# Performance work log

Hardware: AMD Instinct MI355X
Metric: run time of the kernel (lower is better)

Reference implementation:

```python
import jax, jax.numpy as jnp
import numpy as np

N_HEADS = 16
HEAD_DIM = 64
D_MODEL = N_HEADS * HEAD_DIM  # 1024


def setup_inputs() -> dict:
    key = jax.random.key(0)
    ks = jax.random.split(key, 6)
    B, S, D = 2, 2048, D_MODEL
    s = 0.02
    return {
        "hidden_states": jax.random.normal(ks[0], (B, S, D), jnp.float32),
        "position_bias": jax.random.normal(ks[1], (1, N_HEADS, S, S), jnp.float32),
        "Wq": jax.random.normal(ks[2], (D, D), jnp.float32) * s,
        "Wk": jax.random.normal(ks[3], (D, D), jnp.float32) * s,
        "Wv": jax.random.normal(ks[4], (D, D), jnp.float32) * s,
        "Wo": jax.random.normal(ks[5], (D, D), jnp.float32) * s,
    }


def reference(hidden_states, position_bias, Wq, Wk, Wv, Wo):
    B, S, D = hidden_states.shape

    def split_heads(x):  # [B,S,D] -> [B,H,S,hd]
        return x.reshape(B, S, N_HEADS, HEAD_DIM).transpose(0, 2, 1, 3)

    q = split_heads(hidden_states @ Wq)
    k = split_heads(hidden_states @ Wk)
    v = split_heads(hidden_states @ Wv)

    # T5 attention: NO 1/sqrt(d) scaling; additive relative-position bias.
    scores = jnp.einsum("bhqd,bhkd->bhqk", q, k) + position_bias
    attn = jax.nn.softmax(scores.astype(jnp.float32), axis=-1).astype(scores.dtype)
    ctx = jnp.einsum("bhqk,bhkd->bhqd", attn, v)
    ctx = ctx.transpose(0, 2, 1, 3).reshape(B, S, D)
    return ctx @ Wo
```

## Files before the change

kernel.cpp:

```cpp
#include <hip/hip_runtime.h>
#include <hip/hip_bf16.h>
#include <stdint.h>

typedef __bf16 bf16_t;
typedef __bf16 bf16x4 __attribute__((ext_vector_type(4)));
typedef __bf16 bf16x8 __attribute__((ext_vector_type(8)));
typedef float  f32x4  __attribute__((ext_vector_type(4)));

#define S_LEN 2048
#define NH    16
#define HD    64
#define DM    1024
#define BATCH 2
#define M_TOT (BATCH * S_LEN)
#define SM_SHIFT 18.0f

__device__ __forceinline__ void gload16(const void* g, void* l) {
    __builtin_amdgcn_global_load_lds(
        (const __attribute__((address_space(1))) unsigned int*)g,
        (__attribute__((address_space(3))) unsigned int*)l, 16, 0, 0);
}

__global__ void convert_h(const float* __restrict__ X, bf16_t* __restrict__ Y, int n) {
    int i = (blockIdx.x * 256 + threadIdx.x) * 4;
    if (i >= n) return;
    float4 v = *(const float4*)(X + i);
    union { bf16_t h[4]; uint2 u; } pk;
    pk.h[0] = (bf16_t)v.x; pk.h[1] = (bf16_t)v.y;
    pk.h[2] = (bf16_t)v.z; pk.h[3] = (bf16_t)v.w;
    *(uint2*)(Y + i) = pk.u;
}

__global__ void convert_transpose_w4(const float* __restrict__ W0, const float* __restrict__ W1,
                                     const float* __restrict__ W2, const float* __restrict__ W3,
                                     bf16_t* __restrict__ D0, bf16_t* __restrict__ D3) {
    __shared__ float tile[32][33];
    const int z = blockIdx.z;
    const float* W = z == 0 ? W0 : z == 1 ? W1 : z == 2 ? W2 : W3;
    bf16_t* Wt = z < 3 ? D0 + (size_t)z * DM * DM : D3;
    const int tid = threadIdx.x;
    const int tx = tid & 31, ty = tid >> 5;
    const int bx = blockIdx.x * 32, by = blockIdx.y * 32;
#pragma unroll
    for (int it = 0; it < 4; ++it)
        tile[ty + it * 8][tx] = W[(size_t)(by + ty + it * 8) * DM + bx + tx];
    __syncthreads();
#pragma unroll
    for (int it = 0; it < 4; ++it)
        Wt[(size_t)(bx + ty + it * 8) * DM + by + tx] = (bf16_t)tile[tx][ty + it * 8];
}

template<int BN, int EPI>
__global__ __launch_bounds__(256)
void gemm_glds(const bf16_t* __restrict__ A, const bf16_t* __restrict__ Bt,
               float* __restrict__ Cf, bf16_t* __restrict__ Qb, bf16_t* __restrict__ Kb,
               bf16_t* __restrict__ Vtb, int M, int N, int K)
{
    constexpr int WN = BN / 2;
    constexpr int NJ = WN / 16;
    constexpr int RB = BN / 32;
    __shared__ bf16_t smem[16640];
    bf16_t* At  = smem;
    bf16_t* Bts = smem + 8192;

    const int tid  = threadIdx.x;
    const int lane = tid & 63;
    const int wave = tid >> 6;
    const int lc = lane & 15;
    const int l4 = lane >> 4;
    const int wr = wave >> 1, wc = wave & 1;
    const int m0 = blockIdx.y * 128;
    const int n0 = blockIdx.x * BN;
    const int srow = tid >> 3;
    const int scol = (tid & 7) * 8;

    f32x4 acc[4][NJ] = {};

    for (int k0 = 0; k0 < K; k0 += 64) {
        __syncthreads();
#pragma unroll
        for (int ro = 0; ro < 4; ++ro)
            gload16(A + (size_t)(m0 + ro * 32 + srow) * K + k0 + scol,
                    At + ro * 2048 + wave * 512);
#pragma unroll
        for (int ro = 0; ro < RB; ++ro)
            gload16(Bt + (size_t)(n0 + ro * 32 + srow) * K + k0 + scol,
                    Bts + ro * 2048 + wave * 512);
        __syncthreads();

        bf16x8 af[2][4], bfr[2][NJ];
#pragma unroll
        for (int kk = 0; kk < 2; ++kk) {
#pragma unroll
            for (int i = 0; i < 4; ++i)
                af[kk][i] = *(const bf16x8*)(At + (wr * 64 + i * 16 + lc) * 64 + kk * 32 + l4 * 8);
#pragma unroll
            for (int j = 0; j < NJ; ++j)
                bfr[kk][j] = *(const bf16x8*)(Bts + (wc * WN + j * 16 + lc) * 64 + kk * 32 + l4 * 8);
        }
#pragma unroll
        for (int kk = 0; kk < 2; ++kk)
#pragma unroll
            for (int i = 0; i < 4; ++i)
#pragma unroll
                for (int j = 0; j < NJ; ++j)
                    acc[i][j] = __builtin_amdgcn_mfma_f32_16x16x32_bf16(af[kk][i], bfr[kk][j], acc[i][j], 0, 0, 0);
    }

    if (EPI == 1) {
#pragma unroll
        for (int i = 0; i < 4; ++i)
#pragma unroll
            for (int j = 0; j < NJ; ++j)
#pragma unroll
                for (int r = 0; r < 4; ++r) {
                    int m = m0 + wr * 64 + i * 16 + l4 * 4 + r;
                    int n = n0 + wc * WN + j * 16 + lc;
                    Cf[(size_t)m * N + n] = acc[i][j][r];
                }
    } else {
        const int sel = n0 >> 10;
        if (sel < 2) {
            bf16_t* Dst = sel == 0 ? Qb : Kb;
#pragma unroll
            for (int i = 0; i < 4; ++i)
#pragma unroll
                for (int j = 0; j < NJ; ++j)
#pragma unroll
                    for (int r = 0; r < 4; ++r) {
                        int m = m0 + wr * 64 + i * 16 + l4 * 4 + r;
                        int n = (n0 & 1023) + wc * WN + j * 16 + lc;
                        int b = m >> 11, s = m & 2047, h = n >> 6, d = n & 63;
                        Dst[(((size_t)(b * NH + h)) * S_LEN + s) * HD + d] = (bf16_t)acc[i][j][r];
                    }
        } else {
            __syncthreads();
            bf16_t* Ct = smem;
#pragma unroll
            for (int i = 0; i < 4; ++i)
#pragma unroll
                for (int j = 0; j < NJ; ++j)
#pragma unroll
                    for (int r = 0; r < 4; ++r) {
                        int ml = wr * 64 + i * 16 + l4 * 4 + r;
                        int nl = wc * WN + j * 16 + lc;
                        Ct[nl * 130 + ml] = (bf16_t)acc[i][j][r];
                    }
            __syncthreads();
            const int rr = tid >> 1, c0 = (tid & 1) * 64;
            const int nn = (n0 - 2048) + rr;
            const int hh = nn >> 6, dd = nn & 63;
            const int bb = m0 >> 11, s0 = m0 & 2047;
            bf16_t* dst = Vtb + (((size_t)(bb * NH + hh)) * HD + dd) * S_LEN + s0 + c0;
            const bf16_t* srcr = Ct + rr * 130 + c0;
#pragma unroll
            for (int u = 0; u < 8; ++u)
                *(uint4*)(dst + u * 8) = *(const uint4*)(srcr + u * 8);
        }
    }
}

__global__ __launch_bounds__(512, 1)
void attn_kernel(const bf16_t* __restrict__ Q, const bf16_t* __restrict__ Kin,
                 const bf16_t* __restrict__ Vt, const float* __restrict__ bias,
                 bf16_t* __restrict__ Ctx)
{
    const int tid  = threadIdx.x;
    const int lane = tid & 63;
    const int wave = tid >> 6;
    const int b    = wave >> 2;
    const int lc = lane & 15;
    const int l4 = lane >> 4;

    const int f   = blockIdx.x;
    const int xcd = f & 7;
    const int kk_ = f >> 3;
    const int h   = xcd * 2 + (kk_ >> 4);
    const int qt  = kk_ & 15;
    const int qw  = qt * 128 + (wave & 3) * 32;

    __shared__ bf16_t Kt[2][2][64 * 64];
    __shared__ bf16_t Vs[2][2][64 * 64];
    __shared__ bf16_t Pt[8][32 * 68];
    bf16_t* Pw = Pt[wave];

    const bf16_t* Qg = Q + (size_t)(b * NH + h) * S_LEN * HD;
    const bf16_t* Kg[2]; const bf16_t* Vg[2];
#pragma unroll
    for (int bb = 0; bb < 2; ++bb) {
        Kg[bb] = Kin + (size_t)(bb * NH + h) * S_LEN * HD;
        Vg[bb] = Vt  + (size_t)(bb * NH + h) * HD * S_LEN;
    }
    const float* Bg = bias + (size_t)h * S_LEN * S_LEN;

    bf16x8 qf[2][2];
#pragma unroll
    for (int i = 0; i < 2; ++i)
#pragma unroll
        for (int kk = 0; kk < 2; ++kk)
            qf[i][kk] = *(const bf16x8*)(Qg + (size_t)(qw + i * 16 + lc) * HD + kk * 32 + l4 * 8);

    f32x4 cacc[2][4] = {};
    float lsum[2] = {};

    const int r0   = lane >> 3;
    const int gsrc = (lane & 7) ^ r0;
    const int R    = wave * 8;

    auto stage = [&](int t, int pbuf) {
        const int kv0 = t * 64;
        gload16(Kg[0] + (size_t)(kv0 + R + r0) * HD + gsrc * 8, &Kt[0][pbuf][R * 64]);
        gload16(Kg[1] + (size_t)(kv0 + R + r0) * HD + gsrc * 8, &Kt[1][pbuf][R * 64]);
        gload16(Vg[0] + (size_t)(R + r0) * S_LEN + kv0 + gsrc * 8, &Vs[0][pbuf][R * 64]);
        gload16(Vg[1] + (size_t)(R + r0) * S_LEN + kv0 + gsrc * 8, &Vs[1][pbuf][R * 64]);
    };

    auto loadbias = [&](int t, f32x4 (&bv)[2][4]) {
        const int kv0 = t * 64;
#pragma unroll
        for (int i = 0; i < 2; ++i)
#pragma unroll
            for (int j = 0; j < 4; ++j) {
                f32x4 v = *(const f32x4*)(Bg + (size_t)(qw + i * 16 + lc) * S_LEN + kv0 + j * 16 + l4 * 4);
                bv[i][j] = v - SM_SHIFT;
            }
    };

    auto round = [&](int t, f32x4 (&bcur)[2][4], f32x4 (&bnext)[2][4]) {
        const int buf = t & 1;
        if (t < 31) {
            stage(t + 1, buf ^ 1);
            __builtin_amdgcn_sched_barrier(0);
            loadbias(t + 1, bnext);
        }
        __builtin_amdgcn_sched_barrier(0);

        f32x4 saT[4][2] = {};
        __builtin_amdgcn_s_setprio(1);
#pragma unroll
        for (int kk = 0; kk < 2; ++kk) {
            bf16x8 kf[4];
#pragma unroll
            for (int j = 0; j < 4; ++j)
                kf[j] = *(const bf16x8*)(&Kt[b][buf][(j * 16 + lc) * 64 + (((kk * 4 + l4) ^ (lc & 7)) * 8)]);
#pragma unroll
            for (int j = 0; j < 4; ++j)
#pragma unroll
                for (int i = 0; i < 2; ++i)
                    saT[j][i] = __builtin_amdgcn_mfma_f32_16x16x32_bf16(kf[j], qf[i][kk], saT[j][i], 0, 0, 0);
        }
        __builtin_amdgcn_s_setprio(0);

#pragma unroll
        for (int i = 0; i < 2; ++i) {
#pragma unroll
            for (int j = 0; j < 4; ++j) {
                f32x4 s = saT[j][i] + bcur[i][j];
                float p0 = __expf(s.x), p1 = __expf(s.y), p2 = __expf(s.z), p3 = __expf(s.w);
                lsum[i] += (p0 + p1) + (p2 + p3);
                bf16x4 pk = {(bf16_t)p0, (bf16_t)p1, (bf16_t)p2, (bf16_t)p3};
                *(bf16x4*)(&Pw[(i * 16 + lc) * 68 + j * 16 + l4 * 4]) = pk;
            }
        }

        __builtin_amdgcn_s_setprio(1);
#pragma unroll
        for (int ks = 0; ks < 2; ++ks) {
            bf16x8 pf[2], vf[4];
#pragma unroll
            for (int i = 0; i < 2; ++i)
                pf[i] = *(const bf16x8*)(&Pw[(i * 16 + lc) * 68 + ks * 32 + l4 * 8]);
#pragma unroll
            for (int jd = 0; jd < 4; ++jd)
                vf[jd] = *(const bf16x8*)(&Vs[b][buf][(jd * 16 + lc) * 64 + (((ks * 4 + l4) ^ (lc & 7)) * 8)]);
#pragma unroll
            for (int i = 0; i < 2; ++i)
#pragma unroll
                for (int jd = 0; jd < 4; ++jd)
                    cacc[i][jd] = __builtin_amdgcn_mfma_f32_16x16x32_bf16(pf[i], vf[jd], cacc[i][jd], 0, 0, 0);
        }
        __builtin_amdgcn_s_setprio(0);

        __builtin_amdgcn_sched_barrier(0);
        asm volatile("s_waitcnt vmcnt(8)" ::: "memory");
        __builtin_amdgcn_s_barrier();
    };

    f32x4 bvA[2][4], bvB[2][4];
    stage(0, 0);
    __builtin_amdgcn_sched_barrier(0);
    loadbias(0, bvA);
    __builtin_amdgcn_sched_barrier(0);
    asm volatile("s_waitcnt vmcnt(8)" ::: "memory");
    __builtin_amdgcn_s_barrier();

    for (int ot = 0; ot < 16; ++ot) {
        round(2 * ot,     bvA, bvB);
        round(2 * ot + 1, bvB, bvA);
    }

#pragma unroll
    for (int i = 0; i < 2; ++i) {
        lsum[i] += __shfl_xor(lsum[i], 16, 64);
        lsum[i] += __shfl_xor(lsum[i], 32, 64);
    }
    float rinv[2][4];
#pragma unroll
    for (int i = 0; i < 2; ++i)
#pragma unroll
        for (int r = 0; r < 4; ++r)
            rinv[i][r] = 1.0f / __shfl(lsum[i], l4 * 4 + r, 16);

    bf16_t* Co = Ctx + (size_t)b * S_LEN * DM + (size_t)h * HD;
#pragma unroll
    for (int i = 0; i < 2; ++i)
#pragma unroll
        for (int r = 0; r < 4; ++r) {
            int qrow = qw + i * 16 + l4 * 4 + r;
#pragma unroll
            for (int jd = 0; jd < 4; ++jd)
                Co[(size_t)qrow * DM + jd * 16 + lc] = (bf16_t)(cacc[i][jd][r] * rinv[i][r]);
        }
}

extern "C" void kernel_launch(void* const* d_in, const int* in_sizes, int n_in,
                              void* d_out, int out_size, void* d_ws, size_t ws_size,
                              hipStream_t stream)
{
    (void)in_sizes; (void)n_in; (void)out_size; (void)ws_size;
    const float* hs   = (const float*)d_in[0];
    const float* bias = (const float*)d_in[1];
    const float* Wq   = (const float*)d_in[2];
    const float* Wk   = (const float*)d_in[3];
    const float* Wv   = (const float*)d_in[4];
    const float* Wo   = (const float*)d_in[5];
    float* out = (float*)d_out;

    char* ws = (char*)d_ws;
    bf16_t* Hbf   = (bf16_t*)(ws);
    bf16_t* Wqkvt = (bf16_t*)(ws + ( 8u << 20));
    bf16_t* Wot   = (bf16_t*)(ws + (14u << 20));
    bf16_t* Qb    = (bf16_t*)(ws + (16u << 20));
    bf16_t* Kb    = (bf16_t*)(ws + (24u << 20));
    bf16_t* Vtb   = (bf16_t*)(ws + (32u << 20));
    bf16_t* Ctx   = (bf16_t*)(ws + (40u << 20));

    convert_h<<<4096, 256, 0, stream>>>(hs, Hbf, M_TOT * DM);
    dim3 tg(32, 32, 4);
    convert_transpose_w4<<<tg, 256, 0, stream>>>(Wq, Wk, Wv, Wo, Wqkvt, Wot);

    dim3 gq(3 * DM / 128, M_TOT / 128);
    gemm_glds<128, 0><<<gq, 256, 0, stream>>>(Hbf, Wqkvt, nullptr, Qb, Kb, Vtb,
                                              M_TOT, 3 * DM, DM);

    attn_kernel<<<256, 512, 0, stream>>>(Qb, Kb, Vtb, bias, Ctx);

    dim3 go(DM / 64, M_TOT / 128);
    gemm_glds<64, 1><<<go, 256, 0, stream>>>(Ctx, Wot, out, nullptr, nullptr, nullptr,
                                             M_TOT, DM, DM);
}
```

Baseline: 210.7 us.

## Stage position bias through LDS via async loads and reuse buffer for P

After: 189.6 us. 10.0% less time.

```diff
diff --git a/kernel.cpp b/kernel.cpp
--- a/kernel.cpp
+++ b/kernel.cpp
@@ -169,6 +169,7 @@
     const int lane = tid & 63;
     const int wave = tid >> 6;
     const int b    = wave >> 2;
+    const int ws   = wave & 3;
     const int lc = lane & 15;
     const int l4 = lane >> 4;
 
@@ -177,12 +178,11 @@
     const int kk_ = f >> 3;
     const int h   = xcd * 2 + (kk_ >> 4);
     const int qt  = kk_ & 15;
-    const int qw  = qt * 128 + (wave & 3) * 32;
+    const int qw  = qt * 128 + ws * 32;
 
     __shared__ bf16_t Kt[2][2][64 * 64];
     __shared__ bf16_t Vs[2][2][64 * 64];
-    __shared__ bf16_t Pt[8][32 * 68];
-    bf16_t* Pw = Pt[wave];
+    __shared__ float  Bs[2][128 * 64];
 
     const bf16_t* Qg = Q + (size_t)(b * NH + h) * S_LEN * HD;
     const bf16_t* Kg[2]; const bf16_t* Vg[2];
@@ -207,7 +207,7 @@
     const int gsrc = (lane & 7) ^ r0;
     const int R    = wave * 8;
 
-    auto stage = [&](int t, int pbuf) {
+    auto stageKV = [&](int t, int pbuf) {
         const int kv0 = t * 64;
         gload16(Kg[0] + (size_t)(kv0 + R + r0) * HD + gsrc * 8, &Kt[0][pbuf][R * 64]);
         gload16(Kg[1] + (size_t)(kv0 + R + r0) * HD + gsrc * 8, &Kt[1][pbuf][R * 64]);
@@ -215,23 +215,28 @@
         gload16(Vg[1] + (size_t)(R + r0) * S_LEN + kv0 + gsrc * 8, &Vs[1][pbuf][R * 64]);
     };
 
-    auto loadbias = [&](int t, f32x4 (&bv)[2][4]) {
+    const int br4 = lane >> 4;
+    const int bcg = lane & 15;
+    auto stageB = [&](int t, int pbuf) {
         const int kv0 = t * 64;
 #pragma unroll
-        for (int i = 0; i < 2; ++i)
-#pragma unroll
-            for (int j = 0; j < 4; ++j) {
-                f32x4 v = *(const f32x4*)(Bg + (size_t)(qw + i * 16 + lc) * S_LEN + kv0 + j * 16 + l4 * 4);
-                bv[i][j] = v - SM_SHIFT;
-            }
+        for (int c = 0; c < 4; ++c) {
+            const int ql = wave * 16 + c * 4 + br4;
+            const int sg = bcg ^ ((c & 1) * 4 + br4);
+            gload16(Bg + (size_t)(qt * 128 + ql) * S_LEN + kv0 + sg * 4,
+                    (char*)&Bs[pbuf][0] + (wave * 4 + c) * 1024);
+        }
     };
 
-    auto round = [&](int t, f32x4 (&bcur)[2][4], f32x4 (&bnext)[2][4]) {
+    stageKV(0, 0);
+    stageB(0, 0);
+    __syncthreads();
+
+    for (int t = 0; t < 32; ++t) {
         const int buf = t & 1;
         if (t < 31) {
-            stage(t + 1, buf ^ 1);
-            __builtin_amdgcn_sched_barrier(0);
-            loadbias(t + 1, bnext);
+            stageKV(t + 1, buf ^ 1);
+            stageB(t + 1, buf ^ 1);
         }
         __builtin_amdgcn_sched_barrier(0);
 
@@ -251,15 +256,32 @@
         }
         __builtin_amdgcn_s_setprio(0);
 
+        f32x4 bv[2][4];
+        const float* Bbuf = &Bs[buf][0];
+#pragma unroll
+        for (int i = 0; i < 2; ++i)
+#pragma unroll
+            for (int j = 0; j < 4; ++j) {
+                const int ql = ws * 32 + i * 16 + lc;
+                bv[i][j] = *(const f32x4*)(Bbuf + ql * 64 + (((4 * j + l4) ^ (lc & 7)) * 4));
+            }
+
+        asm volatile("s_waitcnt lgkmcnt(0)" ::: "memory");
+        __builtin_amdgcn_sched_barrier(0);
+        __builtin_amdgcn_s_barrier();
+        __builtin_amdgcn_sched_barrier(0);
+
+        bf16_t* Pw = (bf16_t*)&Bs[buf][0] + ws * 4096 + b * 2048;
+
 #pragma unroll
         for (int i = 0; i < 2; ++i) {
 #pragma unroll
             for (int j = 0; j < 4; ++j) {
-                f32x4 s = saT[j][i] + bcur[i][j];
+                f32x4 s = (saT[j][i] - SM_SHIFT) + bv[i][j];
                 float p0 = __expf(s.x), p1 = __expf(s.y), p2 = __expf(s.z), p3 = __expf(s.w);
                 lsum[i] += (p0 + p1) + (p2 + p3);
                 bf16x4 pk = {(bf16_t)p0, (bf16_t)p1, (bf16_t)p2, (bf16_t)p3};
-                *(bf16x4*)(&Pw[(i * 16 + lc) * 68 + j * 16 + l4 * 4]) = pk;
+                *(bf16x4*)(Pw + (i * 16 + lc) * 64 + (((2 * j + (l4 >> 1)) ^ (lc & 7)) << 3) + 4 * (l4 & 1)) = pk;
             }
         }
 
@@ -269,7 +291,7 @@
             bf16x8 pf[2], vf[4];
 #pragma unroll
             for (int i = 0; i < 2; ++i)
-                pf[i] = *(const bf16x8*)(&Pw[(i * 16 + lc) * 68 + ks * 32 + l4 * 8]);
+                pf[i] = *(const bf16x8*)(Pw + (i * 16 + lc) * 64 + (((4 * ks + l4) ^ (lc & 7)) << 3));
 #pragma unroll
             for (int jd = 0; jd < 4; ++jd)
                 vf[jd] = *(const bf16x8*)(&Vs[b][buf][(jd * 16 + lc) * 64 + (((ks * 4 + l4) ^ (lc & 7)) * 8)]);
@@ -281,22 +303,7 @@
         }
         __builtin_amdgcn_s_setprio(0);
 
-        __builtin_amdgcn_sched_barrier(0);
-        asm volatile("s_waitcnt vmcnt(8)" ::: "memory");
-        __builtin_amdgcn_s_barrier();
-    };
-
-    f32x4 bvA[2][4], bvB[2][4];
-    stage(0, 0);
-    __builtin_amdgcn_sched_barrier(0);
-    loadbias(0, bvA);
-    __builtin_amdgcn_sched_barrier(0);
-    asm volatile("s_waitcnt vmcnt(8)" ::: "memory");
-    __builtin_amdgcn_s_barrier();
-
-    for (int ot = 0; ot < 16; ++ot) {
-        round(2 * ot,     bvA, bvB);
-        round(2 * ot + 1, bvB, bvA);
+        __syncthreads();
     }
 
 #pragma unroll
```
